# Kernel tuning notes

Hardware: AMD Instinct MI355X
Metric: run time of the kernel (lower is better)

The kernel has to match this reference:

```python
import jax, jax.numpy as jnp
import numpy as np
from jax import lax

B, T, E, H, N_LAYERS = 64, 256, 512, 512, 2


def _lstm_stack(x, params):
    # x: [B, T, in] -> returns full top-layer hidden sequence [T, B, H]
    xs = jnp.swapaxes(x, 0, 1)  # time-major [T, B, in]
    for (Wih, Whh, bih, bhh) in params:
        def step(carry, xt, Wih=Wih, Whh=Whh, bih=bih, bhh=bhh):
            h, c = carry
            gates = xt @ Wih.T + bih + h @ Whh.T + bhh  # [B, 4H]
            i, f, g, o = jnp.split(gates, 4, axis=-1)   # PyTorch gate order i,f,g,o
            i = jax.nn.sigmoid(i)
            f = jax.nn.sigmoid(f)
            g = jnp.tanh(g)
            o = jax.nn.sigmoid(o)
            c = f * c + i * g
            h = o * jnp.tanh(c)
            return (h, c), h
        nb = xs.shape[1]
        hdim = Whh.shape[1]
        init = (jnp.zeros((nb, hdim), xs.dtype), jnp.zeros((nb, hdim), xs.dtype))
        _, xs = lax.scan(step, init, xs)
    return xs  # [T, B, H]


def setup_inputs() -> dict:
    key = jax.random.key(0)
    ks = jax.random.split(key, 16)
    s = 0.04  # ~1/sqrt(H) init scale
    inp = {"text": jax.random.normal(ks[0], (B, T, E), dtype=jnp.float32)}
    # layer 0: input dim E; layer 1: input dim H
    inp["W_ih0"] = jax.random.normal(ks[1], (4 * H, E), dtype=jnp.float32) * s
    inp["W_hh0"] = jax.random.normal(ks[2], (4 * H, H), dtype=jnp.float32) * s
    inp["b_ih0"] = jax.random.normal(ks[3], (4 * H,), dtype=jnp.float32) * s
    inp["b_hh0"] = jax.random.normal(ks[4], (4 * H,), dtype=jnp.float32) * s
    inp["W_ih1"] = jax.random.normal(ks[5], (4 * H, H), dtype=jnp.float32) * s
    inp["W_hh1"] = jax.random.normal(ks[6], (4 * H, H), dtype=jnp.float32) * s
    inp["b_ih1"] = jax.random.normal(ks[7], (4 * H,), dtype=jnp.float32) * s
    inp["b_hh1"] = jax.random.normal(ks[8], (4 * H,), dtype=jnp.float32) * s
    inp["W_lin"] = jax.random.normal(ks[9], (1, 2 * H), dtype=jnp.float32) * s
    inp["b_lin"] = jax.random.normal(ks[10], (1,), dtype=jnp.float32) * s
    return inp


def reference(text, W_ih0, W_hh0, b_ih0, b_hh0, W_ih1, W_hh1, b_ih1, b_hh1, W_lin, b_lin):
    params = [(W_ih0, W_hh0, b_ih0, b_hh0), (W_ih1, W_hh1, b_ih1, b_hh1)]
    out_f = _lstm_stack(text, params)[-1]                       # [B, H] last step, fwd pass
    out_r = _lstm_stack(jnp.flip(text, axis=1), params)[-1]     # [B, H] last step, reversed input (same weights, as in source)
    out = jnp.concatenate([out_f, out_r], axis=1)               # [B, 2H]
    # dropout is identity in eval mode
    return out @ W_lin.T + b_lin                                # [B, 1]
```

## Files before the change

### kernel.cpp

```cpp
#include <hip/hip_runtime.h>
#include <stdint.h>
#include <math.h>

constexpr int HD   = 512;
constexpr int TS   = 256;
constexpr int NB   = 64;
constexpr int MBR  = 128;
constexpr int SLAB = MBR * HD;

typedef __attribute__((ext_vector_type(8))) short bf16x8;
typedef __attribute__((ext_vector_type(4))) float f32x4;

__device__ __forceinline__ unsigned short f2bf(float f){
  union { float f; unsigned u; } v; v.f = f;
  unsigned r = v.u + 0x7fffu + ((v.u >> 16) & 1u);
  return (unsigned short)(r >> 16);
}
__device__ __forceinline__ float fsig(float x){ return 1.f / (1.f + __expf(-x)); }
__device__ __forceinline__ float ftanh(float x){ return 1.f - 2.f / (__expf(2.f * x) + 1.f); }
__device__ __forceinline__ void vdrain(){ asm volatile("s_waitcnt vmcnt(0)" ::: "memory"); }

__device__ __forceinline__ int ld_flag_sc0(const int* p){
  int v;
  asm volatile("global_load_dword %0, %1, off sc0\n\ts_waitcnt vmcnt(0)"
               : "=v"(v) : "v"(p) : "memory");
  return v;
}
__device__ __forceinline__ int ld_flag_sc1(const int* p){
  int v;
  asm volatile("global_load_dword %0, %1, off sc0 sc1\n\ts_waitcnt vmcnt(0)"
               : "=v"(v) : "v"(p) : "memory");
  return v;
}
__device__ __forceinline__ void st_sc1_b32(void* p, int v){
  asm volatile("global_store_dword %0, %1, off sc0 sc1" :: "v"(p), "v"(v) : "memory");
}

#define LD16_DEF(NAME, FLAGS)                                                   \
__device__ __forceinline__ void NAME(const void* p, f32x4* r){                  \
  asm volatile(                                                                 \
    "global_load_dwordx4 %0,  %16, off " FLAGS "\n\t"                           \
    "global_load_dwordx4 %1,  %16, off offset:64 " FLAGS "\n\t"                 \
    "global_load_dwordx4 %2,  %16, off offset:128 " FLAGS "\n\t"                \
    "global_load_dwordx4 %3,  %16, off offset:192 " FLAGS "\n\t"                \
    "global_load_dwordx4 %4,  %16, off offset:256 " FLAGS "\n\t"                \
    "global_load_dwordx4 %5,  %16, off offset:320 " FLAGS "\n\t"                \
    "global_load_dwordx4 %6,  %16, off offset:384 " FLAGS "\n\t"                \
    "global_load_dwordx4 %7,  %16, off offset:448 " FLAGS "\n\t"                \
    "global_load_dwordx4 %8,  %16, off offset:512 " FLAGS "\n\t"                \
    "global_load_dwordx4 %9,  %16, off offset:576 " FLAGS "\n\t"                \
    "global_load_dwordx4 %10, %16, off offset:640 " FLAGS "\n\t"                \
    "global_load_dwordx4 %11, %16, off offset:704 " FLAGS "\n\t"                \
    "global_load_dwordx4 %12, %16, off offset:768 " FLAGS "\n\t"                \
    "global_load_dwordx4 %13, %16, off offset:832 " FLAGS "\n\t"                \
    "global_load_dwordx4 %14, %16, off offset:896 " FLAGS "\n\t"                \
    "global_load_dwordx4 %15, %16, off offset:960 " FLAGS "\n\t"                \
    "s_waitcnt vmcnt(0)"                                                        \
    : "=&v"(r[0]), "=&v"(r[1]), "=&v"(r[2]), "=&v"(r[3]),                       \
      "=&v"(r[4]), "=&v"(r[5]), "=&v"(r[6]), "=&v"(r[7]),                       \
      "=&v"(r[8]), "=&v"(r[9]), "=&v"(r[10]), "=&v"(r[11]),                     \
      "=&v"(r[12]), "=&v"(r[13]), "=&v"(r[14]), "=&v"(r[15])                    \
    : "v"(p) : "memory");                                                       \
}
LD16_DEF(ld16_sc0, "sc0")
LD16_DEF(ld16_sc1, "sc0 sc1")

__global__ void pack_x(const float* __restrict__ text, unsigned short* __restrict__ Xp){
  int idx = blockIdx.x * 256 + threadIdx.x;
  int k   = idx & 511;
  int row = (idx >> 9) & 127;
  int t   = idx >> 16;
  int b   = row & 63;
  int tt  = (row < 64) ? t : (TS - 1 - t);
  Xp[idx] = f2bf(text[((size_t)b * TS + tt) * HD + k]);
}

__global__ __launch_bounds__(512, 1)
void lstm_persist(const unsigned short* __restrict__ Xp,
                  const float* __restrict__ Wih0, const float* __restrict__ Whh0,
                  const float* __restrict__ bih0, const float* __restrict__ bhh0,
                  const float* __restrict__ Wih1, const float* __restrict__ Whh1,
                  const float* __restrict__ bih1, const float* __restrict__ bhh1,
                  unsigned short* __restrict__ h0r,
                  unsigned short* __restrict__ h0x,
                  unsigned short* __restrict__ h1r,
                  float* __restrict__ H1f,
                  int* __restrict__ F,
                  unsigned* __restrict__ claim)
{
  extern __shared__ unsigned short Blds[];
  __shared__ int s_role;

  const int tid = threadIdx.x;
  if (tid == 0){
    unsigned xcc;
    asm volatile("s_getreg_b32 %0, hwreg(HW_REG_XCC_ID)" : "=s"(xcc));
    xcc &= 7u;
    unsigned idx = __hip_atomic_fetch_add(claim + xcc, 1u,
                     __ATOMIC_RELAXED, __HIP_MEMORY_SCOPE_AGENT);
    s_role = (int)((xcc << 5) | (idx & 31u));
  }
  __syncthreads();
  const int role  = s_role;
  const int xcd   = role >> 5;
  const int layer = xcd & 1;
  const int grp   = xcd >> 1;
  const int slice = role & 31;
  const int m0    = grp * 32;
  const int u0    = slice * 16;
  const int wv    = tid >> 6;
  const int l     = tid & 63;
  const int lj    = l & 15;
  const int lk    = l >> 4;
  const int wgrp  = wv & 3;
  const int mi    = wv >> 2;

  int* F0loc = F + (0 + grp) * (TS * 32);
  int* F1loc = F + (4 + grp) * (TS * 32);
  int* F0x   = F + (8 + grp) * (TS * 32);
  int* F1xg  = F + (12 + grp) * (TS * 32);

  const float* Wihl = layer ? Wih1 : Wih0;
  const float* Whhl = layer ? Whh1 : Whh0;
  for (int it = tid; it < 64 * 128; it += 512){
    int c = it >> 7, kg = it & 127;
    int unit = u0 + ((c >> 4) << 2) + ((c & 15) >> 2);
    int gate = c & 3;
    const float* src = (kg < 64) ? (Wihl + (size_t)(gate * HD + unit) * HD + kg * 8)
                                 : (Whhl + (size_t)(gate * HD + unit) * HD + (kg - 64) * 8);
    float4 v0 = ((const float4*)src)[0];
    float4 v1 = ((const float4*)src)[1];
    bf16x8 w;
    w[0] = (short)f2bf(v0.x); w[1] = (short)f2bf(v0.y);
    w[2] = (short)f2bf(v0.z); w[3] = (short)f2bf(v0.w);
    w[4] = (short)f2bf(v1.x); w[5] = (short)f2bf(v1.y);
    w[6] = (short)f2bf(v1.z); w[7] = (short)f2bf(v1.w);
    *(bf16x8*)((char*)Blds + c * 2048 + ((kg ^ (c & 7)) << 4)) = w;
  }

  const int myunit = u0 + (wgrp << 2) + (lj >> 2);
  const int mygate = lj & 3;
  const float bgv  = (layer ? bih1 : bih0)[mygate * HD + myunit]
                   + (layer ? bhh1 : bhh0)[mygate * HD + myunit];
  const int aoff   = (m0 + mi * 16 + lj) * HD + lk * 8;
  const int cboff  = (wgrp * 16 + lj) * 2048;
  const int swz    = lj & 7;

  float cst[4] = {0.f, 0.f, 0.f, 0.f};
  __syncthreads();

  auto ldsB = [&](int kg)->bf16x8 {
    return *(const bf16x8*)((const char*)Blds + cboff + ((kg ^ swz) << 4));
  };
  auto pollwait = [&](const int* pA, bool a1, const int* pB, bool b1){
    const int* fp = (l < 32) ? (pA + l) : (pB + (l - 32));
    const bool s1 = (l < 32) ? a1 : b1;
    for (;;){
      int v = s1 ? ld_flag_sc1(fp) : ld_flag_sc0(fp);
      if (__all(v != 0)) break;
      __builtin_amdgcn_s_sleep(1);
    }
  };
  auto cellstore = [&](const f32x4& aP, const f32x4& aQ,
                       unsigned short* __restrict__ hloc,
                       unsigned short* __restrict__ hx, bool wrF){
    #pragma unroll
    for (int r = 0; r < 4; ++r){
      float v  = aP[r] + aQ[r] + bgv;
      float v1 = __shfl_xor(v, 1);
      float v2 = __shfl_xor(v, 2);
      float v3 = __shfl_xor(v, 3);
      auto pick = [&](int m)->float {
        return m == 0 ? v : (m == 1 ? v1 : (m == 2 ? v2 : v3));
      };
      float gi = pick(mygate);
      float gf = pick(mygate ^ 1);
      float gg = pick(mygate ^ 2);
      float go = pick(mygate ^ 3);
      float i_ = fsig(gi);
      float f_ = fsig(gf);
      float g_ = ftanh(gg);
      float o_ = fsig(go);
      float c  = f_ * cst[r] + i_ * g_;
      cst[r] = c;
      float h  = o_ * ftanh(c);
      int row  = m0 + mi * 16 + lk * 4 + r;
      int hb   = (int)f2bf(h);
      int pb   = __shfl_xor(hb, 4);
      if (mygate == 0){
        hloc[(size_t)row * HD + myunit] = (unsigned short)hb;
        if (wrF) H1f[(size_t)row * HD + myunit] = h;
      }
      if (hx && ((lj & 7) == 0))
        st_sc1_b32((char*)hx + ((size_t)row * HD + myunit) * 2,
                   (hb & 0xffff) | (pb << 16));
    }
  };

  if (layer == 0){
    f32x4 accPre = {0.f, 0.f, 0.f, 0.f};
    #pragma unroll
    for (int kk = 0; kk < 16; ++kk)
      accPre = __builtin_amdgcn_mfma_f32_16x16x32_bf16(
                 *(const bf16x8*)(Xp + aoff + kk * 32), ldsB(kk * 4 + lk), accPre, 0, 0, 0);
    for (int t = 0; t < TS; ++t){
      if (t > 0){
        if (wv == 0){
          bool bp = (t >= 16) && ((t & 7) == 0);
          const int* pA = F0loc + (t - 1) * 32;
          const int* pB = bp ? (F1xg + ((t >> 3) - 2) * 32) : pA;
          pollwait(pA, false, pB, bp);
        }
        __syncthreads();
      }
      f32x4 accPost = {0.f, 0.f, 0.f, 0.f};
      if (t > 0){
        f32x4 raw[16];
        ld16_sc0(h0r + (size_t)((t - 1) & 3) * SLAB + aoff, raw);
        #pragma unroll
        for (int kk = 0; kk < 16; ++kk)
          accPost = __builtin_amdgcn_mfma_f32_16x16x32_bf16(
                      __builtin_bit_cast(bf16x8, raw[kk]), ldsB(64 + kk * 4 + lk),
                      accPost, 0, 0, 0);
      }
      cellstore(accPre, accPost, h0r + (size_t)(t & 3) * SLAB,
                h0x + (size_t)(t & 15) * SLAB, false);
      vdrain();
      __syncthreads();
      if (tid == 0){
        *(volatile int*)(F0loc + t * 32 + slice) = 1;
        st_sc1_b32(F0x + t * 32 + slice, 1);
      }
      if (t + 1 < TS){
        accPre = (f32x4){0.f, 0.f, 0.f, 0.f};
        #pragma unroll
        for (int kk = 0; kk < 16; ++kk)
          accPre = __builtin_amdgcn_mfma_f32_16x16x32_bf16(
                     *(const bf16x8*)(Xp + (size_t)(t + 1) * SLAB + aoff + kk * 32),
                     ldsB(kk * 4 + lk), accPre, 0, 0, 0);
      }
    }
  } else {
    f32x4 accPre = {0.f, 0.f, 0.f, 0.f};
    {
      if (wv == 0) pollwait(F0x, true, F0x, true);
      __syncthreads();
      f32x4 raw[16];
      ld16_sc1(h0x + aoff, raw);
      #pragma unroll
      for (int kk = 0; kk < 16; ++kk)
        accPre = __builtin_amdgcn_mfma_f32_16x16x32_bf16(
                   __builtin_bit_cast(bf16x8, raw[kk]), ldsB(kk * 4 + lk), accPre, 0, 0, 0);
    }
    for (int t = 0; t < TS; ++t){
      if (t > 0){
        if (wv == 0) pollwait(F1loc + (t - 1) * 32, false, F1loc + (t - 1) * 32, false);
        __syncthreads();
      }
      f32x4 accPost = {0.f, 0.f, 0.f, 0.f};
      if (t > 0){
        f32x4 raw[16];
        ld16_sc0(h1r + (size_t)((t - 1) & 3) * SLAB + aoff, raw);
        #pragma unroll
        for (int kk = 0; kk < 16; ++kk)
          accPost = __builtin_amdgcn_mfma_f32_16x16x32_bf16(
                      __builtin_bit_cast(bf16x8, raw[kk]), ldsB(64 + kk * 4 + lk),
                      accPost, 0, 0, 0);
      }
      cellstore(accPre, accPost, h1r + (size_t)(t & 3) * SLAB, nullptr, t == TS - 1);
      vdrain();
      __syncthreads();
      if (tid == 0){
        *(volatile int*)(F1loc + t * 32 + slice) = 1;
        if ((t & 7) == 7) st_sc1_b32(F1xg + (t >> 3) * 32 + slice, 1);
      }
      if (t + 1 < TS){
        if (wv == 0) pollwait(F0x + (t + 1) * 32, true, F0x + (t + 1) * 32, true);
        __syncthreads();
        accPre = (f32x4){0.f, 0.f, 0.f, 0.f};
        f32x4 raw[16];
        ld16_sc1(h0x + (size_t)((t + 1) & 15) * SLAB + aoff, raw);
        #pragma unroll
        for (int kk = 0; kk < 16; ++kk)
          accPre = __builtin_amdgcn_mfma_f32_16x16x32_bf16(
                     __builtin_bit_cast(bf16x8, raw[kk]), ldsB(kk * 4 + lk),
                     accPre, 0, 0, 0);
      }
    }
  }
}

__global__ void final_linear(const float* __restrict__ H1f, const float* __restrict__ Wlin,
                             const float* __restrict__ blin, float* __restrict__ out){
  int b = blockIdx.x, l = threadIdx.x;
  float s = 0.f;
  for (int j = l; j < HD; j += 64) s += H1f[(size_t)b * HD + j]        * Wlin[j];
  for (int j = l; j < HD; j += 64) s += H1f[(size_t)(NB + b) * HD + j] * Wlin[HD + j];
  #pragma unroll
  for (int off = 32; off; off >>= 1) s += __shfl_down(s, off);
  if (l == 0) out[b] = s + blin[0];
}

extern "C" void kernel_launch(void* const* d_in, const int* in_sizes, int n_in,
                              void* d_out, int out_size, void* d_ws, size_t ws_size,
                              hipStream_t stream)
{
  const float* text = (const float*)d_in[0];
  const float* Wih0 = (const float*)d_in[1];
  const float* Whh0 = (const float*)d_in[2];
  const float* bih0 = (const float*)d_in[3];
  const float* bhh0 = (const float*)d_in[4];
  const float* Wih1 = (const float*)d_in[5];
  const float* Whh1 = (const float*)d_in[6];
  const float* bih1 = (const float*)d_in[7];
  const float* bhh1 = (const float*)d_in[8];
  const float* Wlin = (const float*)d_in[9];
  const float* blin = (const float*)d_in[10];

  uint8_t* p = (uint8_t*)d_ws;
  unsigned short* Xp  = (unsigned short*)p; p += (size_t)TS * SLAB * 2;
  unsigned short* h0r = (unsigned short*)p; p += (size_t)4 * SLAB * 2;
  unsigned short* h0x = (unsigned short*)p; p += (size_t)16 * SLAB * 2;
  unsigned short* h1r = (unsigned short*)p; p += (size_t)4 * SLAB * 2;
  float* H1f          = (float*)p;          p += (size_t)SLAB * 4;
  int* F              = (int*)p;            p += (size_t)16 * TS * 32 * 4;
  unsigned* claim     = (unsigned*)p;       p += 256;

  hipMemsetAsync(F, 0, (size_t)16 * TS * 32 * 4 + 256, stream);

  pack_x<<<65536, 256, 0, stream>>>(text, Xp);

  hipFuncSetAttribute((const void*)lstm_persist,
                      hipFuncAttributeMaxDynamicSharedMemorySize, 131072);

  const unsigned short* XpA = Xp;
  unsigned short* h0A = h0r; unsigned short* hxA = h0x; unsigned short* h1A = h1r;
  float* H1fA = H1f; int* FA = F; unsigned* clA = claim;
  void* args[] = {(void*)&XpA,
                  (void*)&Wih0, (void*)&Whh0, (void*)&bih0, (void*)&bhh0,
                  (void*)&Wih1, (void*)&Whh1, (void*)&bih1, (void*)&bhh1,
                  (void*)&h0A, (void*)&hxA, (void*)&h1A, (void*)&H1fA,
                  (void*)&FA, (void*)&clA};
  hipLaunchCooperativeKernel((void*)lstm_persist, dim3(256), dim3(512),
                             args, 131072, stream);

  final_linear<<<NB, 64, 0, stream>>>(H1f, Wlin, blin, (float*)d_out);
}
```

Before: 3.118 ms.

## Drop XCD-aware role claiming and pack kernel; fuse input conversion into persistent LSTM

Removes the pack_x pre-pass and converts text to bf16 inline inside the layer-0 input projection. Role assignment via XCC_ID atomics is replaced by plain blockIdx mapping, and the per-XCD local flags and h buffers are replaced by device-coherent (sc0 sc1) flags and a full-length h0 history buffer. It also adds a poll timeout abort. The aim is to cut the extra kernel and its memory traffic and to let layer 1 run a step-locked schedule that overlaps the h0 and h1 loads. The cost is that layer-local traffic no longer takes advantage of XCD locality, which may slow the per-step recurrence synchronization.

Result: slower. 3.722 ms (+19.4%).

```diff
diff --git a/kernel.cpp b/kernel.cpp
--- a/kernel.cpp
+++ b/kernel.cpp
@@ -1,6 +1,5 @@
 #include <hip/hip_runtime.h>
 #include <stdint.h>
-#include <math.h>
 
 constexpr int HD   = 512;
 constexpr int TS   = 256;
@@ -20,12 +19,6 @@
 __device__ __forceinline__ float ftanh(float x){ return 1.f - 2.f / (__expf(2.f * x) + 1.f); }
 __device__ __forceinline__ void vdrain(){ asm volatile("s_waitcnt vmcnt(0)" ::: "memory"); }
 
-__device__ __forceinline__ int ld_flag_sc0(const int* p){
-  int v;
-  asm volatile("global_load_dword %0, %1, off sc0\n\ts_waitcnt vmcnt(0)"
-               : "=v"(v) : "v"(p) : "memory");
-  return v;
-}
 __device__ __forceinline__ int ld_flag_sc1(const int* p){
   int v;
   asm volatile("global_load_dword %0, %1, off sc0 sc1\n\ts_waitcnt vmcnt(0)"
@@ -36,78 +29,63 @@
   asm volatile("global_store_dword %0, %1, off sc0 sc1" :: "v"(p), "v"(v) : "memory");
 }
 
-#define LD16_DEF(NAME, FLAGS)                                                   \
+#define LD16_DEF(NAME, TAIL)                                                    \
 __device__ __forceinline__ void NAME(const void* p, f32x4* r){                  \
   asm volatile(                                                                 \
-    "global_load_dwordx4 %0,  %16, off " FLAGS "\n\t"                           \
-    "global_load_dwordx4 %1,  %16, off offset:64 " FLAGS "\n\t"                 \
-    "global_load_dwordx4 %2,  %16, off offset:128 " FLAGS "\n\t"                \
-    "global_load_dwordx4 %3,  %16, off offset:192 " FLAGS "\n\t"                \
-    "global_load_dwordx4 %4,  %16, off offset:256 " FLAGS "\n\t"                \
-    "global_load_dwordx4 %5,  %16, off offset:320 " FLAGS "\n\t"                \
-    "global_load_dwordx4 %6,  %16, off offset:384 " FLAGS "\n\t"                \
-    "global_load_dwordx4 %7,  %16, off offset:448 " FLAGS "\n\t"                \
-    "global_load_dwordx4 %8,  %16, off offset:512 " FLAGS "\n\t"                \
-    "global_load_dwordx4 %9,  %16, off offset:576 " FLAGS "\n\t"                \
-    "global_load_dwordx4 %10, %16, off offset:640 " FLAGS "\n\t"                \
-    "global_load_dwordx4 %11, %16, off offset:704 " FLAGS "\n\t"                \
-    "global_load_dwordx4 %12, %16, off offset:768 " FLAGS "\n\t"                \
-    "global_load_dwordx4 %13, %16, off offset:832 " FLAGS "\n\t"                \
-    "global_load_dwordx4 %14, %16, off offset:896 " FLAGS "\n\t"                \
-    "global_load_dwordx4 %15, %16, off offset:960 " FLAGS "\n\t"                \
-    "s_waitcnt vmcnt(0)"                                                        \
+    "global_load_dwordx4 %0,  %16, off sc0 sc1\n\t"                             \
+    "global_load_dwordx4 %1,  %16, off offset:64 sc0 sc1\n\t"                   \
+    "global_load_dwordx4 %2,  %16, off offset:128 sc0 sc1\n\t"                  \
+    "global_load_dwordx4 %3,  %16, off offset:192 sc0 sc1\n\t"                  \
+    "global_load_dwordx4 %4,  %16, off offset:256 sc0 sc1\n\t"                  \
+    "global_load_dwordx4 %5,  %16, off offset:320 sc0 sc1\n\t"                  \
+    "global_load_dwordx4 %6,  %16, off offset:384 sc0 sc1\n\t"                  \
+    "global_load_dwordx4 %7,  %16, off offset:448 sc0 sc1\n\t"                  \
+    "global_load_dwordx4 %8,  %16, off offset:512 sc0 sc1\n\t"                  \
+    "global_load_dwordx4 %9,  %16, off offset:576 sc0 sc1\n\t"                  \
+    "global_load_dwordx4 %10, %16, off offset:640 sc0 sc1\n\t"                  \
+    "global_load_dwordx4 %11, %16, off offset:704 sc0 sc1\n\t"                  \
+    "global_load_dwordx4 %12, %16, off offset:768 sc0 sc1\n\t"                  \
+    "global_load_dwordx4 %13, %16, off offset:832 sc0 sc1\n\t"                  \
+    "global_load_dwordx4 %14, %16, off offset:896 sc0 sc1\n\t"                  \
+    "global_load_dwordx4 %15, %16, off offset:960 sc0 sc1\n\t"                  \
+    TAIL                                                                        \
     : "=&v"(r[0]), "=&v"(r[1]), "=&v"(r[2]), "=&v"(r[3]),                       \
       "=&v"(r[4]), "=&v"(r[5]), "=&v"(r[6]), "=&v"(r[7]),                       \
       "=&v"(r[8]), "=&v"(r[9]), "=&v"(r[10]), "=&v"(r[11]),                     \
       "=&v"(r[12]), "=&v"(r[13]), "=&v"(r[14]), "=&v"(r[15])                    \
     : "v"(p) : "memory");                                                       \
 }
-LD16_DEF(ld16_sc0, "sc0")
-LD16_DEF(ld16_sc1, "sc0 sc1")
-
-__global__ void pack_x(const float* __restrict__ text, unsigned short* __restrict__ Xp){
-  int idx = blockIdx.x * 256 + threadIdx.x;
-  int k   = idx & 511;
-  int row = (idx >> 9) & 127;
-  int t   = idx >> 16;
-  int b   = row & 63;
-  int tt  = (row < 64) ? t : (TS - 1 - t);
-  Xp[idx] = f2bf(text[((size_t)b * TS + tt) * HD + k]);
+LD16_DEF(ld16_sc1,       "s_waitcnt vmcnt(0)")
+LD16_DEF(ld16_sc1_issue, "s_nop 0")
+
+__device__ __forceinline__ bf16x8 pack8(float4 a, float4 b){
+  bf16x8 w;
+  w[0]=(short)f2bf(a.x); w[1]=(short)f2bf(a.y); w[2]=(short)f2bf(a.z); w[3]=(short)f2bf(a.w);
+  w[4]=(short)f2bf(b.x); w[5]=(short)f2bf(b.y); w[6]=(short)f2bf(b.z); w[7]=(short)f2bf(b.w);
+  return w;
 }
 
 __global__ __launch_bounds__(512, 1)
-void lstm_persist(const unsigned short* __restrict__ Xp,
+void lstm_persist(const float* __restrict__ text,
                   const float* __restrict__ Wih0, const float* __restrict__ Whh0,
                   const float* __restrict__ bih0, const float* __restrict__ bhh0,
                   const float* __restrict__ Wih1, const float* __restrict__ Whh1,
                   const float* __restrict__ bih1, const float* __restrict__ bhh1,
-                  unsigned short* __restrict__ h0r,
                   unsigned short* __restrict__ h0x,
                   unsigned short* __restrict__ h1r,
                   float* __restrict__ H1f,
-                  int* __restrict__ F,
-                  unsigned* __restrict__ claim)
+                  int* __restrict__ F)
 {
   extern __shared__ unsigned short Blds[];
-  __shared__ int s_role;
-
-  const int tid = threadIdx.x;
-  if (tid == 0){
-    unsigned xcc;
-    asm volatile("s_getreg_b32 %0, hwreg(HW_REG_XCC_ID)" : "=s"(xcc));
-    xcc &= 7u;
-    unsigned idx = __hip_atomic_fetch_add(claim + xcc, 1u,
-                     __ATOMIC_RELAXED, __HIP_MEMORY_SCOPE_AGENT);
-    s_role = (int)((xcc << 5) | (idx & 31u));
-  }
-  __syncthreads();
-  const int role  = s_role;
-  const int xcd   = role >> 5;
-  const int layer = xcd & 1;
-  const int grp   = xcd >> 1;
-  const int slice = role & 31;
+  __shared__ int s_abort;
+
+  const int wg    = blockIdx.x;
+  const int layer = wg >> 7;
+  const int grp   = (wg >> 5) & 3;
+  const int slice = wg & 31;
   const int m0    = grp * 32;
   const int u0    = slice * 16;
+  const int tid   = threadIdx.x;
   const int wv    = tid >> 6;
   const int l     = tid & 63;
   const int lj    = l & 15;
@@ -115,10 +93,10 @@
   const int wgrp  = wv & 3;
   const int mi    = wv >> 2;
 
-  int* F0loc = F + (0 + grp) * (TS * 32);
-  int* F1loc = F + (4 + grp) * (TS * 32);
-  int* F0x   = F + (8 + grp) * (TS * 32);
-  int* F1xg  = F + (12 + grp) * (TS * 32);
+  if (tid == 0) s_abort = 0;
+
+  int* F0g = F + (0 + grp) * (TS * 32);
+  int* F1g = F + (4 + grp) * (TS * 32);
 
   const float* Wihl = layer ? Wih1 : Wih0;
   const float* Whhl = layer ? Whh1 : Whh0;
@@ -126,16 +104,10 @@
     int c = it >> 7, kg = it & 127;
     int unit = u0 + ((c >> 4) << 2) + ((c & 15) >> 2);
     int gate = c & 3;
-    const float* src = (kg < 64) ? (Wihl + (size_t)(gate * HD + unit) * HD + kg * 8)
-                                 : (Whhl + (size_t)(gate * HD + unit) * HD + (kg - 64) * 8);
-    float4 v0 = ((const float4*)src)[0];
-    float4 v1 = ((const float4*)src)[1];
-    bf16x8 w;
-    w[0] = (short)f2bf(v0.x); w[1] = (short)f2bf(v0.y);
-    w[2] = (short)f2bf(v0.z); w[3] = (short)f2bf(v0.w);
-    w[4] = (short)f2bf(v1.x); w[5] = (short)f2bf(v1.y);
-    w[6] = (short)f2bf(v1.z); w[7] = (short)f2bf(v1.w);
-    *(bf16x8*)((char*)Blds + c * 2048 + ((kg ^ (c & 7)) << 4)) = w;
+    const float* s = (kg < 64) ? (Wihl + (size_t)(gate * HD + unit) * HD + kg * 8)
+                               : (Whhl + (size_t)(gate * HD + unit) * HD + (kg - 64) * 8);
+    *(bf16x8*)((char*)Blds + c * 2048 + ((kg ^ (c & 7)) << 4)) =
+        pack8(((const float4*)s)[0], ((const float4*)s)[1]);
   }
 
   const int myunit = u0 + (wgrp << 2) + (lj >> 2);
@@ -152,18 +124,19 @@
   auto ldsB = [&](int kg)->bf16x8 {
     return *(const bf16x8*)((const char*)Blds + cboff + ((kg ^ swz) << 4));
   };
-  auto pollwait = [&](const int* pA, bool a1, const int* pB, bool b1){
+  auto pollwait = [&](const int* pA, const int* pB){
+    if (*(volatile int*)&s_abort) return;
     const int* fp = (l < 32) ? (pA + l) : (pB + (l - 32));
-    const bool s1 = (l < 32) ? a1 : b1;
+    int it = 0;
     for (;;){
-      int v = s1 ? ld_flag_sc1(fp) : ld_flag_sc0(fp);
+      int v = ld_flag_sc1(fp);
       if (__all(v != 0)) break;
+      if (++it > 2000000){ s_abort = 1; break; }
       __builtin_amdgcn_s_sleep(1);
     }
   };
   auto cellstore = [&](const f32x4& aP, const f32x4& aQ,
-                       unsigned short* __restrict__ hloc,
-                       unsigned short* __restrict__ hx, bool wrF){
+                       unsigned short* __restrict__ hslab, bool wrF){
     #pragma unroll
     for (int r = 0; r < 4; ++r){
       float v  = aP[r] + aQ[r] + bgv;
@@ -187,105 +160,83 @@
       int row  = m0 + mi * 16 + lk * 4 + r;
       int hb   = (int)f2bf(h);
       int pb   = __shfl_xor(hb, 4);
-      if (mygate == 0){
-        hloc[(size_t)row * HD + myunit] = (unsigned short)hb;
-        if (wrF) H1f[(size_t)row * HD + myunit] = h;
-      }
-      if (hx && ((lj & 7) == 0))
-        st_sc1_b32((char*)hx + ((size_t)row * HD + myunit) * 2,
+      if ((lj & 7) == 0)
+        st_sc1_b32((char*)hslab + ((size_t)row * HD + myunit) * 2,
                    (hb & 0xffff) | (pb << 16));
+      if (wrF && mygate == 0)
+        H1f[(size_t)row * HD + myunit] = h;
+    }
+  };
+  auto preX = [&](int t, f32x4& acc){
+    int ar  = m0 + mi * 16 + lj;
+    int b   = ar & 63;
+    int ts2 = (ar < 64) ? t : (TS - 1 - t);
+    const float* src = text + ((size_t)b * TS + ts2) * HD + lk * 8;
+    acc = (f32x4){0.f, 0.f, 0.f, 0.f};
+    #pragma unroll
+    for (int kk = 0; kk < 16; ++kk){
+      const float* s = src + kk * 32;
+      bf16x8 a = pack8(((const float4*)s)[0], ((const float4*)s)[1]);
+      acc = __builtin_amdgcn_mfma_f32_16x16x32_bf16(a, ldsB(kk * 4 + lk), acc, 0, 0, 0);
     }
   };
 
   if (layer == 0){
-    f32x4 accPre = {0.f, 0.f, 0.f, 0.f};
-    #pragma unroll
-    for (int kk = 0; kk < 16; ++kk)
-      accPre = __builtin_amdgcn_mfma_f32_16x16x32_bf16(
-                 *(const bf16x8*)(Xp + aoff + kk * 32), ldsB(kk * 4 + lk), accPre, 0, 0, 0);
+    f32x4 accPre;
+    preX(0, accPre);
     for (int t = 0; t < TS; ++t){
       if (t > 0){
-        if (wv == 0){
-          bool bp = (t >= 16) && ((t & 7) == 0);
-          const int* pA = F0loc + (t - 1) * 32;
-          const int* pB = bp ? (F1xg + ((t >> 3) - 2) * 32) : pA;
-          pollwait(pA, false, pB, bp);
-        }
+        if (wv == 0) pollwait(F0g + (t - 1) * 32, F0g + (t - 1) * 32);
         __syncthreads();
       }
       f32x4 accPost = {0.f, 0.f, 0.f, 0.f};
       if (t > 0){
         f32x4 raw[16];
-        ld16_sc0(h0r + (size_t)((t - 1) & 3) * SLAB + aoff, raw);
+        ld16_sc1(h0x + (size_t)(t - 1) * SLAB + aoff, raw);
         #pragma unroll
         for (int kk = 0; kk < 16; ++kk)
           accPost = __builtin_amdgcn_mfma_f32_16x16x32_bf16(
                       __builtin_bit_cast(bf16x8, raw[kk]), ldsB(64 + kk * 4 + lk),
                       accPost, 0, 0, 0);
       }
-      cellstore(accPre, accPost, h0r + (size_t)(t & 3) * SLAB,
-                h0x + (size_t)(t & 15) * SLAB, false);
+      cellstore(accPre, accPost, h0x + (size_t)t * SLAB, false);
       vdrain();
       __syncthreads();
-      if (tid == 0){
-        *(volatile int*)(F0loc + t * 32 + slice) = 1;
-        st_sc1_b32(F0x + t * 32 + slice, 1);
-      }
-      if (t + 1 < TS){
-        accPre = (f32x4){0.f, 0.f, 0.f, 0.f};
-        #pragma unroll
-        for (int kk = 0; kk < 16; ++kk)
-          accPre = __builtin_amdgcn_mfma_f32_16x16x32_bf16(
-                     *(const bf16x8*)(Xp + (size_t)(t + 1) * SLAB + aoff + kk * 32),
-                     ldsB(kk * 4 + lk), accPre, 0, 0, 0);
-      }
+      if (tid == 0) st_sc1_b32(F0g + t * 32 + slice, 1);
+      if (t + 1 < TS) preX(t + 1, accPre);
     }
   } else {
-    f32x4 accPre = {0.f, 0.f, 0.f, 0.f};
-    {
-      if (wv == 0) pollwait(F0x, true, F0x, true);
+    for (int t = 0; t < TS; ++t){
+      if (wv == 0){
+        const int* pA = (t > 0) ? (F1g + (t - 1) * 32) : (F0g + 0);
+        pollwait(pA, F0g + t * 32);
+      }
       __syncthreads();
-      f32x4 raw[16];
-      ld16_sc1(h0x + aoff, raw);
+      f32x4 rawI[16], rawR[16];
+      if (t > 0){
+        ld16_sc1_issue(h0x + (size_t)t * SLAB + aoff, rawI);
+        ld16_sc1(h1r + (size_t)((t - 1) & 3) * SLAB + aoff, rawR);
+      } else {
+        ld16_sc1(h0x + aoff, rawI);
+      }
+      f32x4 accPre  = {0.f, 0.f, 0.f, 0.f};
+      f32x4 accPost = {0.f, 0.f, 0.f, 0.f};
       #pragma unroll
       for (int kk = 0; kk < 16; ++kk)
         accPre = __builtin_amdgcn_mfma_f32_16x16x32_bf16(
-                   __builtin_bit_cast(bf16x8, raw[kk]), ldsB(kk * 4 + lk), accPre, 0, 0, 0);
-    }
-    for (int t = 0; t < TS; ++t){
-      if (t > 0){
-        if (wv == 0) pollwait(F1loc + (t - 1) * 32, false, F1loc + (t - 1) * 32, false);
-        __syncthreads();
-      }
-      f32x4 accPost = {0.f, 0.f, 0.f, 0.f};
-      if (t > 0){
-        f32x4 raw[16];
-        ld16_sc0(h1r + (size_t)((t - 1) & 3) * SLAB + aoff, raw);
+                   __builtin_bit_cast(bf16x8, rawI[kk]), ldsB(kk * 4 + lk),
+                   accPre, 0, 0, 0);
+      if (t > 0){
         #pragma unroll
         for (int kk = 0; kk < 16; ++kk)
           accPost = __builtin_amdgcn_mfma_f32_16x16x32_bf16(
-                      __builtin_bit_cast(bf16x8, raw[kk]), ldsB(64 + kk * 4 + lk),
+                      __builtin_bit_cast(bf16x8, rawR[kk]), ldsB(64 + kk * 4 + lk),
                       accPost, 0, 0, 0);
       }
-      cellstore(accPre, accPost, h1r + (size_t)(t & 3) * SLAB, nullptr, t == TS - 1);
+      cellstore(accPre, accPost, h1r + (size_t)(t & 3) * SLAB, t == TS - 1);
       vdrain();
       __syncthreads();
-      if (tid == 0){
-        *(volatile int*)(F1loc + t * 32 + slice) = 1;
-        if ((t & 7) == 7) st_sc1_b32(F1xg + (t >> 3) * 32 + slice, 1);
-      }
-      if (t + 1 < TS){
-        if (wv == 0) pollwait(F0x + (t + 1) * 32, true, F0x + (t + 1) * 32, true);
-        __syncthreads();
-        accPre = (f32x4){0.f, 0.f, 0.f, 0.f};
-        f32x4 raw[16];
-        ld16_sc1(h0x + (size_t)((t + 1) & 15) * SLAB + aoff, raw);
-        #pragma unroll
-        for (int kk = 0; kk < 16; ++kk)
-          accPre = __builtin_amdgcn_mfma_f32_16x16x32_bf16(
-                     __builtin_bit_cast(bf16x8, raw[kk]), ldsB(kk * 4 + lk),
-                     accPre, 0, 0, 0);
-      }
+      if (tid == 0) st_sc1_b32(F1g + t * 32 + slice, 1);
     }
   }
 }
@@ -318,29 +269,25 @@
   const float* blin = (const float*)d_in[10];
 
   uint8_t* p = (uint8_t*)d_ws;
-  unsigned short* Xp  = (unsigned short*)p; p += (size_t)TS * SLAB * 2;
-  unsigned short* h0r = (unsigned short*)p; p += (size_t)4 * SLAB * 2;
-  unsigned short* h0x = (unsigned short*)p; p += (size_t)16 * SLAB * 2;
+  unsigned short* h0x = (unsigned short*)p; p += (size_t)TS * SLAB * 2;
   unsigned short* h1r = (unsigned short*)p; p += (size_t)4 * SLAB * 2;
   float* H1f          = (float*)p;          p += (size_t)SLAB * 4;
-  int* F              = (int*)p;            p += (size_t)16 * TS * 32 * 4;
-  unsigned* claim     = (unsigned*)p;       p += 256;
-
-  hipMemsetAsync(F, 0, (size_t)16 * TS * 32 * 4 + 256, stream);
-
-  pack_x<<<65536, 256, 0, stream>>>(text, Xp);
+  int* F              = (int*)p;            p += (size_t)8 * TS * 32 * 4;
+
+  hipMemsetAsync(F, 0, (size_t)8 * TS * 32 * 4, stream);
 
   hipFuncSetAttribute((const void*)lstm_persist,
                       hipFuncAttributeMaxDynamicSharedMemorySize, 131072);
 
-  const unsigned short* XpA = Xp;
-  unsigned short* h0A = h0r; unsigned short* hxA = h0x; unsigned short* h1A = h1r;
-  float* H1fA = H1f; int* FA = F; unsigned* clA = claim;
-  void* args[] = {(void*)&XpA,
-                  (void*)&Wih0, (void*)&Whh0, (void*)&bih0, (void*)&bhh0,
-                  (void*)&Wih1, (void*)&Whh1, (void*)&bih1, (void*)&bhh1,
-                  (void*)&h0A, (void*)&hxA, (void*)&h1A, (void*)&H1fA,
-                  (void*)&FA, (void*)&clA};
+  const float* A0 = text;
+  const float *A1 = Wih0, *A2 = Whh0, *A3 = bih0, *A4 = bhh0;
+  const float *A5 = Wih1, *A6 = Whh1, *A7 = bih1, *A8 = bhh1;
+  unsigned short* B0 = h0x; unsigned short* B1 = h1r;
+  float* B2 = H1f; int* B3 = F;
+  void* args[] = {(void*)&A0,
+                  (void*)&A1, (void*)&A2, (void*)&A3, (void*)&A4,
+                  (void*)&A5, (void*)&A6, (void*)&A7, (void*)&A8,
+                  (void*)&B0, (void*)&B1, (void*)&B2, (void*)&B3};
   hipLaunchCooperativeKernel((void*)lstm_persist, dim3(256), dim3(512),
                              args, 131072, stream);
 
```
